# Optimization experiments

Hardware: AMD Instinct MI355X
Metric: run time of the kernel (lower is better)

Reference implementation:

```python
import jax, jax.numpy as jnp
import numpy as np

THRESHOLD = 0.5
T = 16777216  # 2**24 timesteps
PERIOD = 256  # note every 256 frames
NOTE_LEN = 200  # offset 200 frames after onset


def setup_inputs() -> dict:
    key = jax.random.key(0)
    k_u, k_e = jax.random.split(key)
    u = jax.random.normal(k_u, (T, 2), dtype=jnp.float32)
    e = jax.random.normal(k_e, (T, 2), dtype=jnp.float32)
    phase = jnp.arange(T, dtype=jnp.int32) % PERIOD
    onsets = (phase == 0).astype(jnp.int32)
    offsets = (phase == NOTE_LEN).astype(jnp.int32)
    return {"u": u, "e": e, "onsets": onsets, "offsets": offsets}


def reference(u, e, onsets, offsets):
    # Vectorized equivalent of the sequential mask build: a timestep is inside
    # a note iff the number of onsets seen so far (inclusive) exceeds the
    # number of offsets seen so far (inclusive). Per-note mask columns are
    # disjoint, so the stacked (T, n_notes) mask reduces to this 1D active mask
    # for both the thresholded count and the normalizer sum(mask).
    cum_on = jnp.cumsum(onsets)
    cum_off = jnp.cumsum(offsets)
    active = (cum_on > cum_off).astype(u.dtype)  # (T,)
    u_f0 = u[:, 0]  # x[0].split(1, -1) -> first channel is f0
    e_f0 = e[:, 0]
    diff = jnp.abs(active * (e_f0 - u_f0))  # mask*|e-u| since mask in {0,1}
    loss = jnp.sum((diff > THRESHOLD).astype(u.dtype)) / jnp.sum(active)
    return loss
```

## Files before the change

### kernel.cpp

```cpp
#include <hip/hip_runtime.h>
#include <math.h>

typedef unsigned long long u64;
typedef float vf4 __attribute__((ext_vector_type(4)));

constexpr int T_TOTAL = 16777216;
constexpr int TPB     = 256;
constexpr int SEG     = 2048;
constexpr int NSEG    = T_TOTAL / SEG;
constexpr int NBLK    = NSEG / 4;
constexpr int ITERS   = SEG / 128;
constexpr float THRESHOLD = 0.5f;

__global__ void __launch_bounds__(TPB)
k_segsums(const int2* __restrict__ on2, const int2* __restrict__ off2,
          int* __restrict__ segsums) {
    const int lane = threadIdx.x & 63;
    const int wid  = threadIdx.x >> 6;
    const int seg  = blockIdx.x * 4 + wid;
    const int base = seg * (SEG / 2);
    int s = 0;
    #pragma unroll
    for (int g = 0; g < ITERS / 4; ++g) {
        const int i0 = base + g * 256 + lane;
        int2 a0 = on2[i0];        int2 a1 = on2[i0 + 64];
        int2 a2 = on2[i0 + 128];  int2 a3 = on2[i0 + 192];
        int2 c0 = off2[i0];       int2 c1 = off2[i0 + 64];
        int2 c2 = off2[i0 + 128]; int2 c3 = off2[i0 + 192];
        s += (a0.x + a0.y - c0.x - c0.y) + (a1.x + a1.y - c1.x - c1.y)
           + (a2.x + a2.y - c2.x - c2.y) + (a3.x + a3.y - c3.x - c3.y);
    }
    #pragma unroll
    for (int d = 32; d > 0; d >>= 1) s += __shfl_xor(s, d);
    if (lane == 0) segsums[seg] = s;
}

__global__ void __launch_bounds__(TPB)
k_scan(int* __restrict__ segsums) {
    __shared__ int wsum[4];
    const int lane = threadIdx.x & 63;
    const int wid  = threadIdx.x >> 6;
    int vals[NSEG / TPB];
    const int base = threadIdx.x * (NSEG / TPB);
    int s = 0;
    #pragma unroll
    for (int i = 0; i < NSEG / TPB; i++) { vals[i] = segsums[base + i]; s += vals[i]; }
    int x = s;
    #pragma unroll
    for (int d = 1; d < 64; d <<= 1) {
        int y = __shfl_up(x, d);
        if (lane >= d) x += y;
    }
    if (lane == 63) wsum[wid] = x;
    __syncthreads();
    int wbase = 0;
    #pragma unroll
    for (int w = 0; w < 3; w++) if (w < wid) wbase += wsum[w];
    int ex = wbase + (x - s);
    #pragma unroll
    for (int i = 0; i < NSEG / TPB; i++) { int v = vals[i]; segsums[base + i] = ex; ex += v; }
}

#define PROC(a, c, uv, ev)                                                    \
    {                                                                         \
        u64 be_on  = __ballot((a).x != 0);                                    \
        u64 bo_on  = __ballot((a).y != 0);                                    \
        u64 be_off = __ballot((c).x != 0);                                    \
        u64 bo_off = __ballot((c).y != 0);                                    \
        const int de = __popcll(be_on & le) - __popcll(be_off & le);          \
        const int pe = basep + de + __popcll(bo_on & lt) - __popcll(bo_off & lt); \
        const int po = basep + de + __popcll(bo_on & le) - __popcll(bo_off & le); \
        basep += __popcll(be_on) - __popcll(be_off)                           \
               + __popcll(bo_on) - __popcll(bo_off);                          \
        const int a0 = pe > 0, a1 = po > 0;                                   \
        cact += a0 + a1;                                                      \
        if (a0 && fabsf((ev)[0] - (uv)[0]) > THRESHOLD) cover++;              \
        if (a1 && fabsf((ev)[2] - (uv)[2]) > THRESHOLD) cover++;              \
    }

__global__ void __launch_bounds__(TPB)
k_count(const int2* __restrict__ on2, const int2* __restrict__ off2,
        const vf4* __restrict__ u4, const vf4* __restrict__ e4,
        const int* __restrict__ segpre, int2* __restrict__ partials) {
    const int lane = threadIdx.x & 63;
    const int wid  = threadIdx.x >> 6;
    const int seg  = blockIdx.x * 4 + wid;
    const int base = seg * (SEG / 2);
    const u64 le = (~0ull) >> (63 - lane);
    const u64 lt = le >> 1;

    int basep = segpre[seg];
    int cover = 0, cact = 0;

    #pragma unroll
    for (int g = 0; g < ITERS / 4; ++g) {
        const int i0 = base + g * 256 + lane;
        int2 a0 = on2[i0];        int2 a1 = on2[i0 + 64];
        int2 a2 = on2[i0 + 128];  int2 a3 = on2[i0 + 192];
        int2 c0 = off2[i0];       int2 c1 = off2[i0 + 64];
        int2 c2 = off2[i0 + 128]; int2 c3 = off2[i0 + 192];
        vf4 u0 = __builtin_nontemporal_load(u4 + i0);
        vf4 u1 = __builtin_nontemporal_load(u4 + i0 + 64);
        vf4 u2 = __builtin_nontemporal_load(u4 + i0 + 128);
        vf4 u3 = __builtin_nontemporal_load(u4 + i0 + 192);
        vf4 e0 = __builtin_nontemporal_load(e4 + i0);
        vf4 e1 = __builtin_nontemporal_load(e4 + i0 + 64);
        vf4 e2 = __builtin_nontemporal_load(e4 + i0 + 128);
        vf4 e3 = __builtin_nontemporal_load(e4 + i0 + 192);
        PROC(a0, c0, u0, e0);
        PROC(a1, c1, u1, e1);
        PROC(a2, c2, u2, e2);
        PROC(a3, c3, u3, e3);
    }

    #pragma unroll
    for (int d = 32; d > 0; d >>= 1) {
        cover += __shfl_xor(cover, d);
        cact  += __shfl_xor(cact, d);
    }
    __shared__ int sc[4], sa[4];
    if (lane == 0) { sc[wid] = cover; sa[wid] = cact; }
    __syncthreads();
    if (threadIdx.x == 0)
        partials[blockIdx.x] = make_int2(sc[0] + sc[1] + sc[2] + sc[3],
                                         sa[0] + sa[1] + sa[2] + sa[3]);
}

__global__ void __launch_bounds__(TPB)
k_final(const int2* __restrict__ partials, float* __restrict__ out) {
    const int lane = threadIdx.x & 63;
    const int wid  = threadIdx.x >> 6;
    int c = 0, a = 0;
    for (int i = threadIdx.x; i < NBLK; i += TPB) {
        int2 p = partials[i];
        c += p.x; a += p.y;
    }
    #pragma unroll
    for (int d = 32; d > 0; d >>= 1) {
        c += __shfl_xor(c, d);
        a += __shfl_xor(a, d);
    }
    __shared__ int sc[4], sa[4];
    if (lane == 0) { sc[wid] = c; sa[wid] = a; }
    __syncthreads();
    if (threadIdx.x == 0) {
        float ctot = (float)(sc[0] + sc[1] + sc[2] + sc[3]);
        float atot = (float)(sa[0] + sa[1] + sa[2] + sa[3]);
        out[0] = ctot / atot;
    }
}

extern "C" void kernel_launch(void* const* d_in, const int* in_sizes, int n_in,
                              void* d_out, int out_size, void* d_ws, size_t ws_size,
                              hipStream_t stream) {
    const float* u   = (const float*)d_in[0];
    const float* e   = (const float*)d_in[1];
    const int*   on  = (const int*)d_in[2];
    const int*   off = (const int*)d_in[3];

    int*  segsums  = (int*)d_ws;
    int2* partials = (int2*)(segsums + NSEG);

    k_segsums<<<NBLK, TPB, 0, stream>>>((const int2*)on, (const int2*)off, segsums);
    k_scan<<<1, TPB, 0, stream>>>(segsums);
    k_count<<<NBLK, TPB, 0, stream>>>((const int2*)on, (const int2*)off,
                                      (const vf4*)u, (const vf4*)e,
                                      segsums, partials);
    k_final<<<1, TPB, 0, stream>>>(partials, (float*)d_out);
}
```

Baseline: 89.68 us.

## Stage count-kernel inputs through double-buffered LDS via global_load_lds, larger segments

The counting kernel now copies each wave's on/off/u/e tile straight from global memory into LDS with `global_load_lds`, one 256-timestep tile at a time. It double-buffers the tiles and uses explicit `s_waitcnt vmcnt` so loading the next tile overlaps computing on the current one. Segment size doubles from 2048 to 4096, which halves the number of segments and blocks and lengthens each wave's stream. The aim is to hide memory latency and keep more bytes in flight in a bandwidth-bound pass. In exchange the kernel uses 48KB of LDS per block, which can lower occupancy, and it relies on hand-written wait counts being correct.

```diff
diff --git a/kernel.cpp b/kernel.cpp
--- a/kernel.cpp
+++ b/kernel.cpp
@@ -6,11 +6,17 @@
 
 constexpr int T_TOTAL = 16777216;
 constexpr int TPB     = 256;
-constexpr int SEG     = 2048;
-constexpr int NSEG    = T_TOTAL / SEG;
+constexpr int SEG_W   = 4096;
+constexpr int NSEG    = T_TOTAL / SEG_W;
 constexpr int NBLK    = NSEG / 4;
-constexpr int ITERS   = SEG / 128;
+constexpr int TILE    = 256;
+constexpr int NT      = SEG_W / TILE;
 constexpr float THRESHOLD = 0.5f;
+
+#define GLD16(g, l)                                                           \
+    __builtin_amdgcn_global_load_lds(                                         \
+        (__attribute__((address_space(1))) void*)(g),                         \
+        (__attribute__((address_space(3))) void*)(l), 16, 0, 0)
 
 __global__ void __launch_bounds__(TPB)
 k_segsums(const int2* __restrict__ on2, const int2* __restrict__ off2,
@@ -18,10 +24,10 @@
     const int lane = threadIdx.x & 63;
     const int wid  = threadIdx.x >> 6;
     const int seg  = blockIdx.x * 4 + wid;
-    const int base = seg * (SEG / 2);
+    const int base = seg * (SEG_W / 2);
     int s = 0;
     #pragma unroll
-    for (int g = 0; g < ITERS / 4; ++g) {
+    for (int g = 0; g < (SEG_W / 2) / 256; ++g) {
         const int i0 = base + g * 256 + lane;
         int2 a0 = on2[i0];        int2 a1 = on2[i0 + 64];
         int2 a2 = on2[i0 + 128];  int2 a3 = on2[i0 + 192];
@@ -78,39 +84,57 @@
         if (a1 && fabsf((ev)[2] - (uv)[2]) > THRESHOLD) cover++;              \
     }
 
+#define STAGE(buf, tb)                                                        \
+    {                                                                         \
+        char* d = (char*)&smem[wid][buf][0];                                  \
+        GLD16(on_  + (tb)         + 4 * lane, d);                             \
+        GLD16(off_ + (tb)         + 4 * lane, d + 1024);                      \
+        GLD16(u_   + 2 * (tb)       + 4 * lane, d + 2048);                    \
+        GLD16(u_   + 2 * (tb) + 256 + 4 * lane, d + 3072);                    \
+        GLD16(e_   + 2 * (tb)       + 4 * lane, d + 4096);                    \
+        GLD16(e_   + 2 * (tb) + 256 + 4 * lane, d + 5120);                    \
+    }
+
 __global__ void __launch_bounds__(TPB)
-k_count(const int2* __restrict__ on2, const int2* __restrict__ off2,
-        const vf4* __restrict__ u4, const vf4* __restrict__ e4,
+k_count(const int* __restrict__ on_, const int* __restrict__ off_,
+        const float* __restrict__ u_, const float* __restrict__ e_,
         const int* __restrict__ segpre, int2* __restrict__ partials) {
+    __shared__ int4 smem[4][2][384];
     const int lane = threadIdx.x & 63;
     const int wid  = threadIdx.x >> 6;
     const int seg  = blockIdx.x * 4 + wid;
-    const int base = seg * (SEG / 2);
+    const int sb   = seg * SEG_W;
     const u64 le = (~0ull) >> (63 - lane);
     const u64 lt = le >> 1;
 
     int basep = segpre[seg];
     int cover = 0, cact = 0;
 
-    #pragma unroll
-    for (int g = 0; g < ITERS / 4; ++g) {
-        const int i0 = base + g * 256 + lane;
-        int2 a0 = on2[i0];        int2 a1 = on2[i0 + 64];
-        int2 a2 = on2[i0 + 128];  int2 a3 = on2[i0 + 192];
-        int2 c0 = off2[i0];       int2 c1 = off2[i0 + 64];
-        int2 c2 = off2[i0 + 128]; int2 c3 = off2[i0 + 192];
-        vf4 u0 = __builtin_nontemporal_load(u4 + i0);
-        vf4 u1 = __builtin_nontemporal_load(u4 + i0 + 64);
-        vf4 u2 = __builtin_nontemporal_load(u4 + i0 + 128);
-        vf4 u3 = __builtin_nontemporal_load(u4 + i0 + 192);
-        vf4 e0 = __builtin_nontemporal_load(e4 + i0);
-        vf4 e1 = __builtin_nontemporal_load(e4 + i0 + 64);
-        vf4 e2 = __builtin_nontemporal_load(e4 + i0 + 128);
-        vf4 e3 = __builtin_nontemporal_load(e4 + i0 + 192);
-        PROC(a0, c0, u0, e0);
-        PROC(a1, c1, u1, e1);
-        PROC(a2, c2, u2, e2);
-        PROC(a3, c3, u3, e3);
+    STAGE(0, sb);
+    for (int t = 0; t < NT; ++t) {
+        const int b = t & 1;
+        if (t + 1 < NT) {
+            STAGE(b ^ 1, sb + (t + 1) * TILE);
+            __builtin_amdgcn_sched_barrier(0);
+            asm volatile("s_waitcnt vmcnt(6)" ::: "memory");
+        } else {
+            asm volatile("s_waitcnt vmcnt(0)" ::: "memory");
+        }
+        __builtin_amdgcn_sched_barrier(0);
+
+        const char* cur = (const char*)&smem[wid][b][0];
+        const int2* onp = (const int2*)cur;
+        const int2* ofp = (const int2*)(cur + 1024);
+        const vf4*  up  = (const vf4*)(cur + 2048);
+        const vf4*  ep  = (const vf4*)(cur + 4096);
+        #pragma unroll
+        for (int k = 0; k < 2; ++k) {
+            int2 a  = onp[64 * k + lane];
+            int2 c  = ofp[64 * k + lane];
+            vf4  uv = up[64 * k + lane];
+            vf4  ev = ep[64 * k + lane];
+            PROC(a, c, uv, ev);
+        }
     }
 
     #pragma unroll
@@ -163,8 +187,6 @@
 
     k_segsums<<<NBLK, TPB, 0, stream>>>((const int2*)on, (const int2*)off, segsums);
     k_scan<<<1, TPB, 0, stream>>>(segsums);
-    k_count<<<NBLK, TPB, 0, stream>>>((const int2*)on, (const int2*)off,
-                                      (const vf4*)u, (const vf4*)e,
-                                      segsums, partials);
+    k_count<<<NBLK, TPB, 0, stream>>>(on, off, u, e, segsums, partials);
     k_final<<<1, TPB, 0, stream>>>(partials, (float*)d_out);
 }
```

After: 98.28 us. 1.1x slower.
